# Optimization experiments

Measured on AMD Instinct MI355X. Metric: run time of the kernel, lower is better.

Reference implementation:

```python
import jax, jax.numpy as jnp
import numpy as np
from jax import lax

EPS = 1e-5

def _dsconv(x, dw, pw, g, b, m, v, relu):
    # x: [B,C,H,W]; dw: [C,1,3,3] depthwise; pw: [C,C,1,1] pointwise; eval-mode BN
    C = x.shape[1]
    y = lax.conv_general_dilated(x, dw, (1, 1), 'SAME', feature_group_count=C)
    y = lax.conv_general_dilated(y, pw, (1, 1), 'SAME')
    scale = (g * lax.rsqrt(v + EPS))[None, :, None, None]
    y = y * scale + (b - m * g * lax.rsqrt(v + EPS))[None, :, None, None]
    return jnp.maximum(y, 0.0) if relu else y

def _attention(x, wq, bq, wk, bk, wv, bv, gamma):
    b, c, h, w = x.shape
    n = h * w
    xf = x.reshape(b, c, n)                      # [B,C,N]
    q = jnp.einsum('oc,bcn->bon', wq, xf) + bq[None, :, None]   # [B,C/8,N]
    k = jnp.einsum('oc,bcn->bon', wk, xf) + bk[None, :, None]   # [B,C/8,N]
    v = jnp.einsum('oc,bcn->bon', wv, xf) + bv[None, :, None]   # [B,C,N]
    logits = jnp.einsum('bdm,bdn->bmn', q, k)    # q^T k, [B,N,N]
    attn = jax.nn.softmax(logits, axis=2)
    out = jnp.einsum('bcn,bmn->bcm', v, attn).reshape(b, c, h, w)
    return gamma[0] * out + x

def setup_inputs() -> dict:
    key = jax.random.key(0)
    ks = jax.random.split(key, 20)
    B, C, H, W = 64, 256, 32, 32
    C8 = C // 8
    rn = lambda k, s, sc: (jax.random.normal(k, s, dtype=jnp.float32) * sc)
    return {
        'x': rn(ks[0], (B, C, H, W), 1.0),
        'dw1': rn(ks[1], (C, 1, 3, 3), 0.2),
        'pw1': rn(ks[2], (C, C, 1, 1), 0.06),
        'bn1_g': jax.random.uniform(ks[3], (C,), jnp.float32, 0.5, 1.5),
        'bn1_b': rn(ks[4], (C,), 0.1),
        'bn1_m': rn(ks[5], (C,), 0.1),
        'bn1_v': jax.random.uniform(ks[6], (C,), jnp.float32, 0.5, 1.5),
        'dw2': rn(ks[7], (C, 1, 3, 3), 0.2),
        'pw2': rn(ks[8], (C, C, 1, 1), 0.06),
        'bn2_g': jax.random.uniform(ks[9], (C,), jnp.float32, 0.5, 1.5),
        'bn2_b': rn(ks[10], (C,), 0.1),
        'bn2_m': rn(ks[11], (C,), 0.1),
        'bn2_v': jax.random.uniform(ks[12], (C,), jnp.float32, 0.5, 1.5),
        'wq': rn(ks[13], (C8, C), 0.06),
        'bq': rn(ks[14], (C8,), 0.02),
        'wk': rn(ks[15], (C8, C), 0.06),
        'bk': rn(ks[16], (C8,), 0.02),
        'wv': rn(ks[17], (C, C), 0.06),
        'bv': rn(ks[18], (C,), 0.02),
        'gamma': rn(ks[19], (1,), 0.5),
    }

def reference(x, dw1, pw1, bn1_g, bn1_b, bn1_m, bn1_v,
              dw2, pw2, bn2_g, bn2_b, bn2_m, bn2_v,
              wq, bq, wk, bk, wv, bv, gamma):
    out = _dsconv(x, dw1, pw1, bn1_g, bn1_b, bn1_m, bn1_v, relu=True)
    out = _dsconv(out, dw2, pw2, bn2_g, bn2_b, bn2_m, bn2_v, relu=False)
    out = _attention(out + x, wq, bq, wk, bk, wv, bv, gamma)
    return jnp.maximum(out, 0.0)
```

## Files before the change

### kernel.cpp

```cpp
#include <hip/hip_runtime.h>
#include <cstdint>
#include <cstddef>

#define B_ 64
#define C_ 256
#define N_ 1024
#define LOG2E 1.4426950408889634f

typedef short v8s __attribute__((ext_vector_type(8)));
typedef float v4f __attribute__((ext_vector_type(4)));
typedef unsigned int u32;
typedef unsigned short u16;

#define VMCNT(N) asm volatile("s_waitcnt vmcnt(" #N ")" ::: "memory")
#define LGKM0 asm volatile("s_waitcnt lgkmcnt(0)" ::: "memory")
#define SBAR __builtin_amdgcn_s_barrier()
#define SCHEDB __builtin_amdgcn_sched_barrier(0)

__device__ __forceinline__ float bf2f(u16 u) {
  return __uint_as_float(((u32)u) << 16);
}
__device__ __forceinline__ u16 f2bf(float f) {
  u32 x = __float_as_uint(f);
  x += 0x7fffu + ((x >> 16) & 1u);
  return (u16)(x >> 16);
}
__device__ __forceinline__ u32 pack2(float a, float b) {
  return (u32)f2bf(a) | ((u32)f2bf(b) << 16);
}
__device__ __forceinline__ u32 cvtpk(float lo, float hi) {
  u32 r;
  asm("v_cvt_pk_bf16_f32 %0, %1, %2" : "=v"(r) : "v"(lo), "v"(hi));
  return r;
}

typedef __attribute__((address_space(3))) unsigned int lds_as_t;
typedef __attribute__((address_space(1))) const unsigned int glb_as_t;
__device__ __forceinline__ void ld_lds16(const u16* g, u16* l) {
  __builtin_amdgcn_global_load_lds((glb_as_t*)g, (lds_as_t*)l, 16, 0, 0);
}

__global__ __launch_bounds__(256) void prep(
    const float* __restrict__ g1, const float* __restrict__ b1,
    const float* __restrict__ m1, const float* __restrict__ v1,
    const float* __restrict__ g2, const float* __restrict__ b2,
    const float* __restrict__ m2, const float* __restrict__ v2,
    const float* __restrict__ wq, const float* __restrict__ bq,
    const float* __restrict__ wk, const float* __restrict__ bk,
    const float* __restrict__ wv, const float* __restrict__ bv,
    const float* __restrict__ pw1, const float* __restrict__ pw2,
    const float* __restrict__ dw1, const float* __restrict__ dw2,
    float* __restrict__ scale1, float* __restrict__ shift1,
    float* __restrict__ scale2, float* __restrict__ shift2,
    float* __restrict__ dwT1, float* __restrict__ dwT2,
    u16* __restrict__ pw1b, u16* __restrict__ pw2b, u16* __restrict__ wcatb,
    float* __restrict__ bcat) {
  const int gt = blockIdx.x * 256 + threadIdx.x;
  if (gt < 256) {
    float s1 = g1[gt] * rsqrtf(v1[gt] + 1e-5f);
    scale1[gt] = s1;
    shift1[gt] = b1[gt] - m1[gt] * s1;
    float s2 = g2[gt] * rsqrtf(v2[gt] + 1e-5f);
    scale2[gt] = s2;
    shift2[gt] = b2[gt] - m2[gt] * s2;
  }
  if (gt < 320)
    bcat[gt] = (gt < 32) ? bq[gt] * LOG2E
                         : (gt < 64) ? bk[gt - 32] : bv[gt - 64];
  if (gt < 2304) {
    dwT1[(gt % 9) * 256 + gt / 9] = dw1[gt];
    dwT2[(gt % 9) * 256 + gt / 9] = dw2[gt];
  }
  for (int e = gt; e < 65536; e += 16384) {
    pw1b[e] = f2bf(pw1[e]);
    pw2b[e] = f2bf(pw2[e]);
  }
  for (int e = gt; e < 81920; e += 16384) {
    const int o = e >> 8;
    float w = (o < 32) ? wq[e] * LOG2E
                       : (o < 64) ? wk[e - 8192] : wv[e - 16384];
    wcatb[e] = f2bf(w);
  }
}

__global__ __launch_bounds__(256) void transpose_x(const float* __restrict__ x,
                                                   u16* __restrict__ xt) {
  __shared__ float t[64][65];
  const int b = blockIdx.z, c0 = blockIdx.y * 64, n0 = blockIdx.x * 64;
  const float* xp = x + ((size_t)b * C_ + c0) * N_ + n0;
  const int tn = threadIdx.x & 63, tc = threadIdx.x >> 6;
#pragma unroll
  for (int i = 0; i < 16; ++i)
    t[tc + 4 * i][tn] = xp[(size_t)(tc + 4 * i) * N_ + tn];
  __syncthreads();
  u16* op = xt + ((size_t)b * N_ + n0) * C_ + c0;
  const int oc = threadIdx.x & 63, on = threadIdx.x >> 6;
#pragma unroll
  for (int i = 0; i < 16; ++i)
    op[(size_t)(on + 4 * i) * C_ + oc] = f2bf(t[oc][on + 4 * i]);
}

__global__ __launch_bounds__(256) void dw_nhwc(const u16* __restrict__ src,
                                               const float* __restrict__ wT,
                                               u16* __restrict__ dst) {
  __shared__ float wl[9][256];
  const int b = blockIdx.y;
  for (int e = threadIdx.x; e < 2304; e += 256) wl[e >> 8][e & 255] = wT[e];
  __syncthreads();
  const int pl = threadIdx.x >> 5, c0 = (threadIdx.x & 31) * 8;
  const int p = blockIdx.x * 8 + pl;
  const int h = p >> 5, wx = p & 31;
  const u16* sp = src + (size_t)b * N_ * C_;
  float acc[8] = {0.f, 0.f, 0.f, 0.f, 0.f, 0.f, 0.f, 0.f};
#pragma unroll
  for (int dh = -1; dh <= 1; ++dh) {
    const int hh = h + dh;
    if (hh < 0 || hh > 31) continue;
#pragma unroll
    for (int dx = -1; dx <= 1; ++dx) {
      const int ww = wx + dx;
      if (ww < 0 || ww > 31) continue;
      const int k = (dh + 1) * 3 + (dx + 1);
      const uint4 v = *(const uint4*)(sp + (size_t)(hh * 32 + ww) * C_ + c0);
      const u32 vv[4] = {v.x, v.y, v.z, v.w};
#pragma unroll
      for (int j = 0; j < 4; ++j) {
        acc[2 * j] += bf2f((u16)(vv[j] & 0xffffu)) * wl[k][c0 + 2 * j];
        acc[2 * j + 1] += bf2f((u16)(vv[j] >> 16)) * wl[k][c0 + 2 * j + 1];
      }
    }
  }
  uint4 o4;
  o4.x = pack2(acc[0], acc[1]);
  o4.y = pack2(acc[2], acc[3]);
  o4.z = pack2(acc[4], acc[5]);
  o4.w = pack2(acc[6], acc[7]);
  *(uint4*)(dst + ((size_t)b * N_ + p) * C_ + c0) = o4;
}

template <int EPI>
__global__ __launch_bounds__(256) void gemm(
    const u16* __restrict__ X, const u16* __restrict__ W,
    const float* __restrict__ scale, const float* __restrict__ shift,
    const u16* __restrict__ resid, u16* __restrict__ Y, u16* __restrict__ Y2) {
  __shared__ u16 smem[32768];
  u16(*Ys)[136] = (u16(*)[136])smem;
  u16(*YsQ)[68] = (u16(*)[68])smem;

  const int tid = threadIdx.x;
  const int b = blockIdx.z;
  const int n0 = blockIdx.x * 128, o0 = blockIdx.y * 128;
  const int wid = tid >> 6, lane = tid & 63;
  const int wn = wid & 1, wo = wid >> 1;
  const int l15 = lane & 15, l4 = lane >> 4;
  const int lr = lane >> 3, lc = (lane & 7) * 8;

  v4f acc[4][4];
#pragma unroll
  for (int i = 0; i < 4; ++i)
#pragma unroll
    for (int j = 0; j < 4; ++j) acc[i][j] = v4f{0.f, 0.f, 0.f, 0.f};

  auto stage = [&](int kidx, int bufsel) {
    const int k0 = (kidx & 3) * 64;
    u16* Xd = smem + bufsel * 16384;
    u16* Wd = smem + bufsel * 16384 + 8192;
#pragma unroll
    for (int g = 0; g < 4; ++g) {
      const int base = wid * 32 + g * 8;
      ld_lds16(X + ((size_t)b * N_ + n0 + base + lr) * C_ + k0 + lc,
               Xd + base * 64);
      int wr = o0 + base + lr;
      if (EPI == 2 && wr > 319) wr = 319;
      ld_lds16(W + (size_t)wr * C_ + k0 + lc, Wd + base * 64);
    }
  };

  stage(0, 0);
  stage(1, 1);

#pragma unroll
  for (int k = 0; k < 4; ++k) {
    const int cur = k & 1;
    if (k < 3) {
      VMCNT(8);
    } else {
      VMCNT(0);
    }
    SCHEDB;
    SBAR;
    const u16(*Xs)[64] = (const u16(*)[64])(smem + cur * 16384);
    const u16(*Ws)[64] = (const u16(*)[64])(smem + cur * 16384 + 8192);
#pragma unroll
    for (int ks = 0; ks < 2; ++ks) {
      v8s af[4], bf4[4];
#pragma unroll
      for (int f = 0; f < 4; ++f) {
        if constexpr (EPI != 2) {
          af[f] = *(const v8s*)&Ws[wo * 64 + f * 16 + l15][ks * 32 + l4 * 8];
          bf4[f] = *(const v8s*)&Xs[wn * 64 + f * 16 + l15][ks * 32 + l4 * 8];
        } else {
          af[f] = *(const v8s*)&Xs[wn * 64 + f * 16 + l15][ks * 32 + l4 * 8];
          bf4[f] = *(const v8s*)&Ws[wo * 64 + f * 16 + l15][ks * 32 + l4 * 8];
        }
      }
#pragma unroll
      for (int i = 0; i < 4; ++i)
#pragma unroll
        for (int j = 0; j < 4; ++j)
          acc[i][j] = __builtin_amdgcn_mfma_f32_16x16x32_bf16(
              af[i], bf4[j], acc[i][j], 0, 0, 0);
    }
    LGKM0;
    SBAR;
    SCHEDB;
    if (k < 2) stage(k + 2, cur);
  }

  if constexpr (EPI != 2) {
#pragma unroll
    for (int i = 0; i < 4; ++i) {
      const int oL = wo * 64 + i * 16 + l4 * 4;
      const int o = o0 + oL;
      const float4 sc = *(const float4*)&scale[o];
      const float4 sh = *(const float4*)&shift[o];
#pragma unroll
      for (int j = 0; j < 4; ++j) {
        const int nL = wn * 64 + j * 16 + l15;
        float y0 = acc[i][j][0] * sc.x + sh.x;
        float y1 = acc[i][j][1] * sc.y + sh.y;
        float y2 = acc[i][j][2] * sc.z + sh.z;
        float y3 = acc[i][j][3] * sc.w + sh.w;
        if constexpr (EPI == 0) {
          y0 = fmaxf(y0, 0.f);
          y1 = fmaxf(y1, 0.f);
          y2 = fmaxf(y2, 0.f);
          y3 = fmaxf(y3, 0.f);
        } else {
          const uint2 rb =
              *(const uint2*)(resid + ((size_t)b * N_ + n0 + nL) * C_ + o);
          y0 += bf2f((u16)(rb.x & 0xffffu));
          y1 += bf2f((u16)(rb.x >> 16));
          y2 += bf2f((u16)(rb.y & 0xffffu));
          y3 += bf2f((u16)(rb.y >> 16));
        }
        uint2 st;
        st.x = pack2(y0, y1);
        st.y = pack2(y2, y3);
        *(uint2*)&Ys[nL][oL] = st;
      }
    }
    __syncthreads();
#pragma unroll
    for (int s = 0; s < 8; ++s) {
      const int nL = s * 16 + (tid >> 4);
      const int slot = tid & 15;
      const uint4 v = *(const uint4*)&Ys[nL][slot * 8];
      *(uint4*)&Y[((size_t)b * N_ + n0 + nL) * C_ + o0 + slot * 8] = v;
    }
  } else {
    float bj[4];
#pragma unroll
    for (int j = 0; j < 4; ++j) {
      int o = o0 + wo * 64 + j * 16 + l15;
      bj[j] = shift[o > 319 ? 319 : o];
    }
    if (o0 == 0 && wo == 0) {
#pragma unroll
      for (int i = 0; i < 4; ++i) {
        const int nL = wn * 64 + i * 16 + l4 * 4;
#pragma unroll
        for (int j = 0; j < 4; ++j) {
          const int oL = j * 16 + l15;
#pragma unroll
          for (int r = 0; r < 4; ++r)
            YsQ[nL + r][oL] = f2bf(acc[i][j][r] + bj[j]);
        }
      }
    } else {
#pragma unroll
      for (int i = 0; i < 4; ++i) {
        const int nL = wn * 64 + i * 16 + l4 * 4;
#pragma unroll
        for (int j = 0; j < 4; ++j) {
          const int oL = wo * 64 + j * 16 + l15;
          uint2 st;
          st.x = pack2(acc[i][j][0] + bj[j], acc[i][j][1] + bj[j]);
          st.y = pack2(acc[i][j][2] + bj[j], acc[i][j][3] + bj[j]);
          *(uint2*)&Ys[oL][nL] = st;
        }
      }
    }
    __syncthreads();
    if (o0 == 0) {
#pragma unroll
      for (int s = 0; s < 4; ++s) {
        const int e = s * 256 + tid;
        const int row = e >> 3, seg = e & 7;
        const uint4 v = *(const uint4*)&YsQ[row][seg * 8];
        *(uint4*)&Y[((size_t)b * N_ + n0 + row) * 64 + seg * 8] = v;
      }
#pragma unroll
      for (int s = 0; s < 4; ++s) {
        const int e = s * 256 + tid;
        const int oL = 64 + (e >> 4), slot = e & 15;
        const uint4 v = *(const uint4*)&Ys[oL][slot * 8];
        *(uint4*)&Y2[((size_t)b * C_ + oL - 64) * N_ + n0 + slot * 8] = v;
      }
    } else {
#pragma unroll
      for (int s = 0; s < 8; ++s) {
        const int oL = s * 16 + (tid >> 4);
        const int c = o0 + oL - 64;
        if (c < 256) {
          const int slot = tid & 15;
          const uint4 v = *(const uint4*)&Ys[oL][slot * 8];
          *(uint4*)&Y2[((size_t)b * C_ + c) * N_ + n0 + slot * 8] = v;
        }
      }
    }
  }
}

__global__ __launch_bounds__(256, 3) void flash(
    const u16* __restrict__ qk, const u16* __restrict__ vchw,
    const u16* __restrict__ abf, const float* __restrict__ gamma_p,
    float* __restrict__ out) {
  const int b = blockIdx.x;
  const int m0 = blockIdx.y * 64;
  const int tid = threadIdx.x, wid = tid >> 6, lane = tid & 63;
  const int l15 = lane & 15, l4 = lane >> 4;
  const int mw = m0 + wid * 16;
  const int cq = wid * 64;

  __shared__ u16 Vs[256][64];
  __shared__ u16 Pl[2][64][72];
  __shared__ float Sl[64];

  const u16* qkb = qk + (size_t)b * N_ * 64;
  const u16* vb = vchw + (size_t)b * C_ * N_;
  const v8s qf = *(const v8s*)&qkb[(size_t)(mw + l15) * 64 + l4 * 8];

  const int s_row = lane >> 3;
  const int s_j = (lane & 7) ^ (s_row & 7);

#pragma unroll
  for (int g = 0; g < 8; ++g) {
    const int base = cq + g * 8;
    ld_lds16(vb + (size_t)(base + s_row) * N_ + s_j * 8, &Vs[base][0]);
  }

  float Mloc = -3e38f;
  {
    v8s kf[4];
#pragma unroll
    for (int f = 0; f < 4; ++f)
      kf[f] = *(const v8s*)&qkb[(size_t)(f * 16 + l15) * 64 + 32 + l4 * 8];
    for (int t = 0; t < 16; ++t) {
      v8s kn[4];
      if (t < 15) {
        const int n1 = (t + 1) * 64;
#pragma unroll
        for (int f = 0; f < 4; ++f)
          kn[f] =
              *(const v8s*)&qkb[(size_t)(n1 + f * 16 + l15) * 64 + 32 + l4 * 8];
      }
#pragma unroll
      for (int f = 0; f < 4; ++f) {
        const v4f lt = __builtin_amdgcn_mfma_f32_16x16x32_bf16(
            kf[f], qf, v4f{0.f, 0.f, 0.f, 0.f}, 0, 0, 0);
        Mloc = fmaxf(Mloc, fmaxf(fmaxf(lt[0], lt[1]), fmaxf(lt[2], lt[3])));
      }
      if (t < 15) {
#pragma unroll
        for (int f = 0; f < 4; ++f) kf[f] = kn[f];
      }
    }
  }
  Mloc = fmaxf(Mloc, __shfl_xor(Mloc, 16));
  Mloc = fmaxf(Mloc, __shfl_xor(Mloc, 32));
  const float M = Mloc;

  v4f acc[4][4];
#pragma unroll
  for (int mf = 0; mf < 4; ++mf)
#pragma unroll
    for (int j = 0; j < 4; ++j) acc[mf][j] = v4f{0.f, 0.f, 0.f, 0.f};
  float S0 = 0.f, S1 = 0.f, S2 = 0.f, S3 = 0.f;
  v8s kf[4];
#pragma unroll
  for (int f = 0; f < 4; ++f)
    kf[f] = *(const v8s*)&qkb[(size_t)(f * 16 + l15) * 64 + 32 + l4 * 8];
  VMCNT(0);

  for (int t = 0; t < 16; ++t) {
    const int tb = t & 1;
    v4f lt[4];
#pragma unroll
    for (int f = 0; f < 4; ++f)
      lt[f] = __builtin_amdgcn_mfma_f32_16x16x32_bf16(
          kf[f], qf, v4f{0.f, 0.f, 0.f, 0.f}, 0, 0, 0);
#pragma unroll
    for (int f = 0; f < 4; ++f) {
      const float p0 = exp2f(lt[f][0] - M);
      const float p1 = exp2f(lt[f][1] - M);
      const float p2 = exp2f(lt[f][2] - M);
      const float p3 = exp2f(lt[f][3] - M);
      S0 += p0;
      S1 += p1;
      S2 += p2;
      S3 += p3;
      uint2 pw;
      pw.x = cvtpk(p0, p1);
      pw.y = cvtpk(p2, p3);
      *(uint2*)&Pl[tb][wid * 16 + l15][f * 16 + l4 * 4] = pw;
    }
    SCHEDB;
    {
      const int n1 = ((t + 1) & 15) * 64;
#pragma unroll
      for (int f = 0; f < 4; ++f)
        kf[f] =
            *(const v8s*)&qkb[(size_t)(n1 + f * 16 + l15) * 64 + 32 + l4 * 8];
    }
    SCHEDB;
    LGKM0;
    SBAR;
    VMCNT(4);
    SCHEDB;
    __builtin_amdgcn_s_setprio(1);
#pragma unroll
    for (int ks = 0; ks < 2; ++ks) {
      v8s pa[4];
#pragma unroll
      for (int mf = 0; mf < 4; ++mf)
        pa[mf] = *(const v8s*)&Pl[tb][mf * 16 + l15][ks * 32 + l4 * 8];
#pragma unroll
      for (int j = 0; j < 4; ++j) {
        const int col = 8 * (((ks * 4) + l4) ^ (l15 & 7));
        const v8s vf = *(const v8s*)&Vs[cq + j * 16 + l15][col];
#pragma unroll
        for (int mf = 0; mf < 4; ++mf)
          acc[mf][j] = __builtin_amdgcn_mfma_f32_16x16x32_bf16(
              pa[mf], vf, acc[mf][j], 0, 0, 0);
      }
    }
    __builtin_amdgcn_s_setprio(0);
    SCHEDB;
    {
      const int n1 = ((t + 1) & 15) * 64;
#pragma unroll
      for (int g = 0; g < 8; ++g) {
        const int base = cq + g * 8;
        ld_lds16(vb + (size_t)(base + s_row) * N_ + n1 + s_j * 8, &Vs[base][0]);
      }
    }
    SCHEDB;
  }

  float S = (S0 + S1) + (S2 + S3);
  S += __shfl_xor(S, 16);
  S += __shfl_xor(S, 32);
  if (lane < 16) Sl[wid * 16 + lane] = 1.f / S;
  __syncthreads();

  const float gma = gamma_p[0];
  float invv[4][4];
#pragma unroll
  for (int mf = 0; mf < 4; ++mf)
#pragma unroll
    for (int r = 0; r < 4; ++r) invv[mf][r] = Sl[mf * 16 + l4 * 4 + r];

#pragma unroll
  for (int mf = 0; mf < 4; ++mf) {
    const int mb = m0 + mf * 16 + l4 * 4;
#pragma unroll
    for (int j = 0; j < 4; ++j) {
      const int c = cq + j * 16 + l15;
      float4 y;
      float* yp = (float*)&y;
#pragma unroll
      for (int r = 0; r < 4; ++r) {
        const float av = bf2f(abf[((size_t)b * N_ + mb + r) * C_ + c]);
        yp[r] = fmaxf(gma * acc[mf][j][r] * invv[mf][r] + av, 0.f);
      }
      *(float4*)&out[((size_t)b * C_ + c) * N_ + mb] = y;
    }
  }
}

extern "C" void kernel_launch(void* const* d_in, const int* in_sizes, int n_in,
                              void* d_out, int out_size, void* d_ws,
                              size_t ws_size, hipStream_t stream) {
  const float* x = (const float*)d_in[0];
  const float* dw1 = (const float*)d_in[1];
  const float* pw1 = (const float*)d_in[2];
  const float* bn1g = (const float*)d_in[3];
  const float* bn1b = (const float*)d_in[4];
  const float* bn1m = (const float*)d_in[5];
  const float* bn1v = (const float*)d_in[6];
  const float* dw2 = (const float*)d_in[7];
  const float* pw2 = (const float*)d_in[8];
  const float* bn2g = (const float*)d_in[9];
  const float* bn2b = (const float*)d_in[10];
  const float* bn2m = (const float*)d_in[11];
  const float* bn2v = (const float*)d_in[12];
  const float* wq = (const float*)d_in[13];
  const float* bq = (const float*)d_in[14];
  const float* wk = (const float*)d_in[15];
  const float* bk = (const float*)d_in[16];
  const float* wv = (const float*)d_in[17];
  const float* bv = (const float*)d_in[18];
  const float* gamma = (const float*)d_in[19];
  float* out = (float*)d_out;

  char* ws = (char*)d_ws;
  size_t off = 0;
  auto alloc = [&](size_t bytes) {
    void* p = ws + off;
    off += (bytes + 255) & ~(size_t)255;
    return p;
  };
  const size_t NE = (size_t)B_ * N_ * C_;

  u16* bufA = (u16*)alloc(NE * 2);
  u16* bufB = (u16*)alloc(NE * 2);
  u16* bufC = (u16*)alloc(NE * 2);
  u16* abf = (u16*)alloc(NE * 2);
  float* scale1 = (float*)alloc(256 * 4);
  float* shift1 = (float*)alloc(256 * 4);
  float* scale2 = (float*)alloc(256 * 4);
  float* shift2 = (float*)alloc(256 * 4);
  float* dwT1 = (float*)alloc(2304 * 4);
  float* dwT2 = (float*)alloc(2304 * 4);
  u16* pw1b = (u16*)alloc(65536 * 2);
  u16* pw2b = (u16*)alloc(65536 * 2);
  u16* wcatb = (u16*)alloc(81920 * 2);
  float* bcat = (float*)alloc(384 * 4);

  u16* xt = bufA;
  u16* t1 = bufB;
  u16* y1 = bufC;
  u16* t2 = bufB;
  u16* qkbuf = bufC;
  u16* vchw = bufA;

  prep<<<64, 256, 0, stream>>>(bn1g, bn1b, bn1m, bn1v, bn2g, bn2b, bn2m, bn2v,
                               wq, bq, wk, bk, wv, bv, pw1, pw2, dw1, dw2,
                               scale1, shift1, scale2, shift2, dwT1, dwT2,
                               pw1b, pw2b, wcatb, bcat);
  transpose_x<<<dim3(16, 4, B_), 256, 0, stream>>>(x, xt);
  dw_nhwc<<<dim3(128, B_), 256, 0, stream>>>(xt, dwT1, t1);
  gemm<0><<<dim3(8, 2, B_), 256, 0, stream>>>(t1, pw1b, scale1, shift1,
                                              nullptr, y1, nullptr);
  dw_nhwc<<<dim3(128, B_), 256, 0, stream>>>(y1, dwT2, t2);
  gemm<1><<<dim3(8, 2, B_), 256, 0, stream>>>(t2, pw2b, scale2, shift2, xt,
                                              abf, nullptr);
  gemm<2><<<dim3(8, 3, B_), 256, 0, stream>>>(abf, wcatb, nullptr, bcat,
                                              nullptr, qkbuf, vchw);
  flash<<<dim3(64, 16), 256, 0, stream>>>(qkbuf, vchw, abf, gamma, out);
}
```

Before: 256.3 us.

## Split flash attention into stats pass and channel-split PV pass

The fused flash kernel is replaced by two kernels. A stats kernel computes the online row max and log-sum-exp for each query row. A PV kernel then uses that precomputed normaliser and splits the 256 output channels across two blocks in z. This doubles the grid to 2048 blocks and halves the accumulator and LDS per block, which lets occupancy rise to 4 blocks per unit and removes the final normalisation. In exchange, the QK^T logits and exp are recomputed in each channel-half block, and an extra launch plus a small madj buffer are added.

```diff
diff --git a/kernel.cpp b/kernel.cpp
--- a/kernel.cpp
+++ b/kernel.cpp
@@ -322,71 +322,101 @@
   }
 }
 
-__global__ __launch_bounds__(256, 3) void flash(
-    const u16* __restrict__ qk, const u16* __restrict__ vchw,
-    const u16* __restrict__ abf, const float* __restrict__ gamma_p,
-    float* __restrict__ out) {
+__global__ __launch_bounds__(256) void attn_stats(const u16* __restrict__ qk,
+                                                  float* __restrict__ madj) {
   const int b = blockIdx.x;
   const int m0 = blockIdx.y * 64;
   const int tid = threadIdx.x, wid = tid >> 6, lane = tid & 63;
   const int l15 = lane & 15, l4 = lane >> 4;
   const int mw = m0 + wid * 16;
-  const int cq = wid * 64;
-
-  __shared__ u16 Vs[256][64];
+  const u16* qkb = qk + (size_t)b * N_ * 64;
+  const v8s qf = *(const v8s*)&qkb[(size_t)(mw + l15) * 64 + l4 * 8];
+
+  float M = -3e38f, S = 0.f;
+  v8s kf[4];
+#pragma unroll
+  for (int f = 0; f < 4; ++f)
+    kf[f] = *(const v8s*)&qkb[(size_t)(f * 16 + l15) * 64 + 32 + l4 * 8];
+  for (int t = 0; t < 16; ++t) {
+    v8s kn[4];
+    if (t < 15) {
+      const int n1 = (t + 1) * 64;
+#pragma unroll
+      for (int f = 0; f < 4; ++f)
+        kn[f] =
+            *(const v8s*)&qkb[(size_t)(n1 + f * 16 + l15) * 64 + 32 + l4 * 8];
+    }
+    v4f lt[4];
+#pragma unroll
+    for (int f = 0; f < 4; ++f)
+      lt[f] = __builtin_amdgcn_mfma_f32_16x16x32_bf16(
+          kf[f], qf, v4f{0.f, 0.f, 0.f, 0.f}, 0, 0, 0);
+    float pmax = -3e38f;
+#pragma unroll
+    for (int f = 0; f < 4; ++f)
+#pragma unroll
+      for (int r = 0; r < 4; ++r) pmax = fmaxf(pmax, lt[f][r]);
+    const float Mn = fmaxf(M, pmax);
+    float sum = 0.f;
+#pragma unroll
+    for (int f = 0; f < 4; ++f) {
+      const float p0 = exp2f(lt[f][0] - Mn);
+      const float p1 = exp2f(lt[f][1] - Mn);
+      const float p2 = exp2f(lt[f][2] - Mn);
+      const float p3 = exp2f(lt[f][3] - Mn);
+      sum += (p0 + p1) + (p2 + p3);
+    }
+    S = S * exp2f(M - Mn) + sum;
+    M = Mn;
+    if (t < 15) {
+#pragma unroll
+      for (int f = 0; f < 4; ++f) kf[f] = kn[f];
+    }
+  }
+#pragma unroll
+  for (int off = 16; off <= 32; off <<= 1) {
+    const float Mo = __shfl_xor(M, off);
+    const float So = __shfl_xor(S, off);
+    const float Mn = fmaxf(M, Mo);
+    S = S * exp2f(M - Mn) + So * exp2f(Mo - Mn);
+    M = Mn;
+  }
+  if (l4 == 0) madj[(size_t)b * N_ + mw + l15] = M + __log2f(S);
+}
+
+__global__ __launch_bounds__(256, 4) void attn_pv(
+    const u16* __restrict__ qk, const u16* __restrict__ vchw,
+    const u16* __restrict__ abf, const float* __restrict__ madj,
+    const float* __restrict__ gamma_p, float* __restrict__ out) {
+  const int b = blockIdx.x;
+  const int m0 = blockIdx.y * 64;
+  const int ch0 = blockIdx.z * 128;
+  const int tid = threadIdx.x, wid = tid >> 6, lane = tid & 63;
+  const int l15 = lane & 15, l4 = lane >> 4;
+  const int mw = m0 + wid * 16;
+  const int cqL = wid * 32;
+
+  __shared__ u16 Vs[128][64];
   __shared__ u16 Pl[2][64][72];
-  __shared__ float Sl[64];
 
   const u16* qkb = qk + (size_t)b * N_ * 64;
-  const u16* vb = vchw + (size_t)b * C_ * N_;
+  const u16* vb = vchw + (size_t)b * C_ * N_ + (size_t)ch0 * N_;
   const v8s qf = *(const v8s*)&qkb[(size_t)(mw + l15) * 64 + l4 * 8];
+  const float mdj = madj[(size_t)b * N_ + mw + l15];
 
   const int s_row = lane >> 3;
   const int s_j = (lane & 7) ^ (s_row & 7);
 
 #pragma unroll
-  for (int g = 0; g < 8; ++g) {
-    const int base = cq + g * 8;
+  for (int g = 0; g < 4; ++g) {
+    const int base = cqL + g * 8;
     ld_lds16(vb + (size_t)(base + s_row) * N_ + s_j * 8, &Vs[base][0]);
   }
-
-  float Mloc = -3e38f;
-  {
-    v8s kf[4];
-#pragma unroll
-    for (int f = 0; f < 4; ++f)
-      kf[f] = *(const v8s*)&qkb[(size_t)(f * 16 + l15) * 64 + 32 + l4 * 8];
-    for (int t = 0; t < 16; ++t) {
-      v8s kn[4];
-      if (t < 15) {
-        const int n1 = (t + 1) * 64;
-#pragma unroll
-        for (int f = 0; f < 4; ++f)
-          kn[f] =
-              *(const v8s*)&qkb[(size_t)(n1 + f * 16 + l15) * 64 + 32 + l4 * 8];
-      }
-#pragma unroll
-      for (int f = 0; f < 4; ++f) {
-        const v4f lt = __builtin_amdgcn_mfma_f32_16x16x32_bf16(
-            kf[f], qf, v4f{0.f, 0.f, 0.f, 0.f}, 0, 0, 0);
-        Mloc = fmaxf(Mloc, fmaxf(fmaxf(lt[0], lt[1]), fmaxf(lt[2], lt[3])));
-      }
-      if (t < 15) {
-#pragma unroll
-        for (int f = 0; f < 4; ++f) kf[f] = kn[f];
-      }
-    }
-  }
-  Mloc = fmaxf(Mloc, __shfl_xor(Mloc, 16));
-  Mloc = fmaxf(Mloc, __shfl_xor(Mloc, 32));
-  const float M = Mloc;
-
-  v4f acc[4][4];
+  v4f acc[4][2];
 #pragma unroll
   for (int mf = 0; mf < 4; ++mf)
 #pragma unroll
-    for (int j = 0; j < 4; ++j) acc[mf][j] = v4f{0.f, 0.f, 0.f, 0.f};
-  float S0 = 0.f, S1 = 0.f, S2 = 0.f, S3 = 0.f;
+    for (int j = 0; j < 2; ++j) acc[mf][j] = v4f{0.f, 0.f, 0.f, 0.f};
   v8s kf[4];
 #pragma unroll
   for (int f = 0; f < 4; ++f)
@@ -402,14 +432,10 @@
           kf[f], qf, v4f{0.f, 0.f, 0.f, 0.f}, 0, 0, 0);
 #pragma unroll
     for (int f = 0; f < 4; ++f) {
-      const float p0 = exp2f(lt[f][0] - M);
-      const float p1 = exp2f(lt[f][1] - M);
-      const float p2 = exp2f(lt[f][2] - M);
-      const float p3 = exp2f(lt[f][3] - M);
-      S0 += p0;
-      S1 += p1;
-      S2 += p2;
-      S3 += p3;
+      const float p0 = exp2f(lt[f][0] - mdj);
+      const float p1 = exp2f(lt[f][1] - mdj);
+      const float p2 = exp2f(lt[f][2] - mdj);
+      const float p3 = exp2f(lt[f][3] - mdj);
       uint2 pw;
       pw.x = cvtpk(p0, p1);
       pw.y = cvtpk(p2, p3);
@@ -436,9 +462,9 @@
       for (int mf = 0; mf < 4; ++mf)
         pa[mf] = *(const v8s*)&Pl[tb][mf * 16 + l15][ks * 32 + l4 * 8];
 #pragma unroll
-      for (int j = 0; j < 4; ++j) {
+      for (int j = 0; j < 2; ++j) {
         const int col = 8 * (((ks * 4) + l4) ^ (l15 & 7));
-        const v8s vf = *(const v8s*)&Vs[cq + j * 16 + l15][col];
+        const v8s vf = *(const v8s*)&Vs[cqL + j * 16 + l15][col];
 #pragma unroll
         for (int mf = 0; mf < 4; ++mf)
           acc[mf][j] = __builtin_amdgcn_mfma_f32_16x16x32_bf16(
@@ -450,39 +476,27 @@
     {
       const int n1 = ((t + 1) & 15) * 64;
 #pragma unroll
-      for (int g = 0; g < 8; ++g) {
-        const int base = cq + g * 8;
+      for (int g = 0; g < 4; ++g) {
+        const int base = cqL + g * 8;
         ld_lds16(vb + (size_t)(base + s_row) * N_ + n1 + s_j * 8, &Vs[base][0]);
       }
     }
     SCHEDB;
   }
 
-  float S = (S0 + S1) + (S2 + S3);
-  S += __shfl_xor(S, 16);
-  S += __shfl_xor(S, 32);
-  if (lane < 16) Sl[wid * 16 + lane] = 1.f / S;
-  __syncthreads();
-
   const float gma = gamma_p[0];
-  float invv[4][4];
-#pragma unroll
-  for (int mf = 0; mf < 4; ++mf)
-#pragma unroll
-    for (int r = 0; r < 4; ++r) invv[mf][r] = Sl[mf * 16 + l4 * 4 + r];
-
 #pragma unroll
   for (int mf = 0; mf < 4; ++mf) {
     const int mb = m0 + mf * 16 + l4 * 4;
 #pragma unroll
-    for (int j = 0; j < 4; ++j) {
-      const int c = cq + j * 16 + l15;
+    for (int j = 0; j < 2; ++j) {
+      const int c = ch0 + cqL + j * 16 + l15;
       float4 y;
       float* yp = (float*)&y;
 #pragma unroll
       for (int r = 0; r < 4; ++r) {
         const float av = bf2f(abf[((size_t)b * N_ + mb + r) * C_ + c]);
-        yp[r] = fmaxf(gma * acc[mf][j][r] * invv[mf][r] + av, 0.f);
+        yp[r] = fmaxf(gma * acc[mf][j][r] + av, 0.f);
       }
       *(float4*)&out[((size_t)b * C_ + c) * N_ + mb] = y;
     }
@@ -527,6 +541,7 @@
   u16* bufB = (u16*)alloc(NE * 2);
   u16* bufC = (u16*)alloc(NE * 2);
   u16* abf = (u16*)alloc(NE * 2);
+  float* madj = (float*)alloc((size_t)B_ * N_ * 4);
   float* scale1 = (float*)alloc(256 * 4);
   float* shift1 = (float*)alloc(256 * 4);
   float* scale2 = (float*)alloc(256 * 4);
@@ -558,5 +573,7 @@
                                               abf, nullptr);
   gemm<2><<<dim3(8, 3, B_), 256, 0, stream>>>(abf, wcatb, nullptr, bcat,
                                               nullptr, qkbuf, vchw);
-  flash<<<dim3(64, 16), 256, 0, stream>>>(qkbuf, vchw, abf, gamma, out);
-}
+  attn_stats<<<dim3(64, 16), 256, 0, stream>>>(qkbuf, madj);
+  attn_pv<<<dim3(64, 16, 2), 256, 0, stream>>>(qkbuf, vchw, abf, madj, gamma,
+                                               out);
+}
```

Result: slower. 279.7 us (+9.1%).
